# Kernel optimization log

Measured on AMD Instinct MI355X. Metric: run time of the kernel, lower is better.

Reference implementation:

```python
import jax, jax.numpy as jnp
import numpy as np

T, B, FEAT, HID, NCLS = 256, 64, 256, 1024, 257


def hamilton_block(W):
    # W: [4, di, do] components (r,i,j,k) -> full real block matrix [4*di, 4*do]
    Wr, Wi, Wj, Wk = W[0], W[1], W[2], W[3]
    row0 = jnp.concatenate([Wr, Wi, Wj, Wk], axis=-1)
    row1 = jnp.concatenate([-Wi, Wr, -Wk, Wj], axis=-1)
    row2 = jnp.concatenate([-Wj, Wk, Wr, -Wi], axis=-1)
    row3 = jnp.concatenate([-Wk, -Wj, Wi, Wr], axis=-1)
    return jnp.concatenate([row0, row1, row2, row3], axis=-2)


def setup_inputs() -> dict:
    key = jax.random.key(0)
    ks = jax.random.split(key, 7)
    x = jax.random.normal(ks[0], (T, B, FEAT), dtype=jnp.float32)
    sx = 1.0 / np.sqrt(FEAT)
    sh = 1.0 / np.sqrt(HID)
    # 4 gates (f,i,o,c) x 4 quaternion components x [feat/4, hid/4]
    Wx = jax.random.normal(ks[1], (4, 4, FEAT // 4, HID // 4), dtype=jnp.float32) * sx
    bx = jax.random.normal(ks[2], (4, HID), dtype=jnp.float32) * sx
    Wh = jax.random.normal(ks[3], (4, 4, HID // 4, HID // 4), dtype=jnp.float32) * sh
    Wo = jax.random.normal(ks[4], (HID, NCLS), dtype=jnp.float32) * sh
    bo = jax.random.normal(ks[5], (NCLS,), dtype=jnp.float32) * sh
    return {"x": x, "Wx": Wx, "bx": bx, "Wh": Wh, "Wo": Wo, "bo": bo}


def reference(x, Wx, bx, Wh, Wo, bo):
    # Build full real Hamilton-product matrices per gate.
    Wx_full = jax.vmap(hamilton_block)(Wx)  # [4, FEAT, HID]
    Wh_full = jax.vmap(hamilton_block)(Wh)  # [4, HID, HID]
    # Precompute input-to-hidden gate terms for all timesteps: [4, T, B, HID]
    gx = jnp.einsum('tbf,gfh->gtbh', x, Wx_full) + bx[:, None, None, :]

    def step(carry, gx_t):  # gx_t: [4, B, HID]
        h, c = carry
        gh = jnp.einsum('bh,gho->gbo', h, Wh_full)  # [4, B, HID]
        ft = jax.nn.sigmoid(gx_t[0] + gh[0])
        it = jax.nn.sigmoid(gx_t[1] + gh[1])
        ot = jax.nn.sigmoid(gx_t[2] + gh[2])
        at = gx_t[3] + gh[3]
        c = it * jnp.tanh(at) + ft * c
        h = ot * jnp.tanh(c)
        return (h, c), h

    h0 = jnp.zeros((B, HID), dtype=x.dtype)
    _, hs = jax.lax.scan(step, (h0, h0), jnp.moveaxis(gx, 1, 0))  # hs: [T, B, HID]
    return jnp.einsum('tbh,hc->tbc', hs, Wo) + bo  # [T, B, NCLS]
```

## Files before the change

kernel.cpp:

```cpp
#include <hip/hip_runtime.h>
#include <hip/hip_bf16.h>
#include <math.h>

#define T 256
#define B 64
#define FEAT 256
#define HID 1024
#define NCLS 257
#define NCH 4
#define NCG 64
#define NBLK 256
#define NTHR 512
#define HSLOT 16384
#define XSLOT 4096

typedef __attribute__((ext_vector_type(8))) short short8v;
typedef __attribute__((ext_vector_type(4))) float floatx4;

__device__ __constant__ int   d_comp[4][4] = {{0,1,2,3},{1,0,3,2},{2,3,0,1},{3,2,1,0}};
__device__ __constant__ float d_sign[4][4] = {{ 1.f, 1.f, 1.f, 1.f},
                                              {-1.f, 1.f,-1.f, 1.f},
                                              {-1.f, 1.f, 1.f,-1.f},
                                              {-1.f,-1.f, 1.f, 1.f}};

__device__ __forceinline__ ushort f2bf(float f) {
    union { float f; unsigned u; } v; v.f = f;
    unsigned r = v.u + 0x7FFF + ((v.u >> 16) & 1);
    return (ushort)(r >> 16);
}

__device__ __forceinline__ float sigm(float v) { return 1.f / (1.f + __expf(-v)); }
__device__ __forceinline__ float tanh_fast(float v) { return 1.f - 2.f / (1.f + __expf(2.f * v)); }

__global__ __launch_bounds__(256) void conv_xpanel(const float* __restrict__ x,
                                                   ushort* __restrict__ xp) {
    int i = blockIdx.x * 256 + threadIdx.x;
    int k4 = i & 63, b = (i >> 6) & 63, t = i >> 12;
    int k = k4 * 4;
    int c = b >> 4, b16 = b & 15;
    float4 v = ((const float4*)x)[i];
    ushort4 o;
    o.x = f2bf(v.x); o.y = f2bf(v.y); o.z = f2bf(v.z); o.w = f2bf(v.w);
    *(ushort4*)(xp + (size_t)(t * 4 + c) * XSLOT + (k >> 3) * 128 + b16 * 8 + (k & 7)) = o;
}

__global__ __launch_bounds__(256) void prep_wcf(const float* __restrict__ Wh,
                                                const float* __restrict__ Wx,
                                                ushort* __restrict__ wcf) {
    int e = blockIdx.x * 256 + threadIdx.x;
    int j    = e & 7;
    int lane = (e >> 3) & 63;
    int r    = e >> 9;
    int ks   = r % 40;
    int s    = r / 40;
    int mt   = s & 3;
    int cg   = s >> 2;
    int c  = mt * 16 + (lane & 15);
    int hl = c >> 2, g = c & 3;
    int n  = cg * 16 + hl;
    int qq = n >> 8, bc = n & 255;
    int k  = ks * 32 + ((lane >> 4) << 3) + j;
    float v;
    if (k < HID) {
        int p = k >> 8, a = k & 255;
        v = d_sign[p][qq] * Wh[((g * 4 + d_comp[p][qq]) * 256 + a) * 256 + bc];
    } else {
        int kk = k - HID;
        int p = kk >> 6, a = kk & 63;
        v = d_sign[p][qq] * Wx[((g * 4 + d_comp[p][qq]) * 64 + a) * 256 + bc];
    }
    wcf[e] = f2bf(v);
}

__global__ __launch_bounds__(256) void prep_wof(const float* __restrict__ Wo,
                                                ushort* __restrict__ wof) {
    int e = blockIdx.x * 256 + threadIdx.x;
    int j    = e & 7;
    int lane = (e >> 3) & 63;
    int ks   = (e >> 9) & 31;
    int tile = e >> 14;
    int n = tile * 16 + (lane & 15);
    int k = ks * 32 + ((lane >> 4) << 3) + j;
    wof[e] = (n < NCLS) ? f2bf(Wo[k * NCLS + n]) : (ushort)0;
}

__global__ __launch_bounds__(256) void init_hf(ushort* __restrict__ hpan,
                                               uint* __restrict__ flg) {
    int i = blockIdx.x * 256 + threadIdx.x;
    ((ushort4*)hpan)[i] = make_ushort4(0, 0, 0, 0);
    if (blockIdx.x == 0) flg[threadIdx.x] = 0;
}

__global__ __launch_bounds__(512, 2) void qlstm_persist(
    const ushort* __restrict__ xp,
    const ushort* __restrict__ wcf,
    const float*  __restrict__ bx,
    ushort*       __restrict__ hpan,
    uint*         __restrict__ flg)
{
    __shared__ float pre[2][16][72];

    const int tid  = threadIdx.x;
    const int blk  = blockIdx.x;
    const int ch   = blk & 3;
    const int cg   = blk >> 2;
    const int w    = tid >> 6;
    const int lane = tid & 63;
    const int mt   = w & 3;
    const int kh   = w >> 2;
    const int ld_off = (lane >> 4) * 128 + (lane & 15) * 8;

    const ushort* wbase = wcf + ((size_t)(cg * 4 + mt) * 40 + kh * 20) * 512 + lane * 8;
    short8v A[20];
    #pragma unroll
    for (int i = 0; i < 20; ++i) {
        const ushort* ap = wbase + i * 512;
        asm volatile("global_load_dwordx4 %0, %1, off" : "=v"(A[i]) : "v"(ap));
    }
    asm volatile("s_waitcnt vmcnt(0)" ::: "memory");
    __builtin_amdgcn_sched_barrier(0);

    const int gb = tid >> 4;
    const int hl = tid & 15;
    const int gn = cg * 16 + hl;
    float bxf = 0.f, bxi = 0.f, bxo = 0.f, bxa = 0.f;
    if (tid < 256) {
        bxf = bx[gn]; bxi = bx[HID + gn];
        bxo = bx[2 * HID + gn]; bxa = bx[3 * HID + gn];
    }
    float c_reg = 0.f;
    const int st_off = (cg * 2 + (hl >> 3)) * 128 + gb * 8 + (hl & 7);
    uint* myflags = flg + ch * 64;

    for (int t = 0; t < T; ++t) {
        const ushort* hs = hpan + (size_t)(t * NCH + ch) * HSLOT;
        const ushort* xs = xp   + (size_t)(t * NCH + ch) * XSLOT;

        short8v Bf[20];
        if (kh == 1) {
            #pragma unroll
            for (int i = 12; i < 20; ++i) {
                const ushort* p = xs + (i - 12) * 512 + ld_off;
                asm volatile("global_load_dwordx4 %0, %1, off" : "=v"(Bf[i]) : "v"(p));
            }
        }

        if (t > 0) {
            if (w == 0) {
                const uint tgt = (uint)t;
                for (;;) {
                    uint f = __hip_atomic_load(myflags + lane, __ATOMIC_RELAXED,
                                               __HIP_MEMORY_SCOPE_AGENT);
                    if (__all(f >= tgt)) break;
                    __builtin_amdgcn_s_sleep(1);
                }
            }
            __syncthreads();
        }

        if (kh == 0) {
            #pragma unroll
            for (int i = 0; i < 20; ++i) {
                const ushort* p = hs + i * 512 + ld_off;
                asm volatile("global_load_dwordx4 %0, %1, off" : "=v"(Bf[i]) : "v"(p));
            }
        } else {
            #pragma unroll
            for (int i = 0; i < 12; ++i) {
                const ushort* p = hs + (20 + i) * 512 + ld_off;
                asm volatile("global_load_dwordx4 %0, %1, off" : "=v"(Bf[i]) : "v"(p));
            }
        }
        asm volatile("s_waitcnt vmcnt(0)" ::: "memory");
        __builtin_amdgcn_sched_barrier(0);

        floatx4 a0 = {0.f,0.f,0.f,0.f}, a1 = {0.f,0.f,0.f,0.f};
        #pragma unroll
        for (int i = 0; i < 20; i += 2) {
            a0 = __builtin_amdgcn_mfma_f32_16x16x32_bf16(A[i],     Bf[i],     a0, 0, 0, 0);
            a1 = __builtin_amdgcn_mfma_f32_16x16x32_bf16(A[i + 1], Bf[i + 1], a1, 0, 0, 0);
        }
        floatx4 acc = a0 + a1;

        {
            float4 v = make_float4(acc[0], acc[1], acc[2], acc[3]);
            *(float4*)&pre[kh][lane & 15][mt * 16 + (lane >> 4) * 4] = v;
        }
        __syncthreads();

        if (tid < 256) {
            float4 p0 = *(const float4*)&pre[0][gb][hl * 4];
            float4 p1 = *(const float4*)&pre[1][gb][hl * 4];
            float f  = sigm(p0.x + p1.x + bxf);
            float i_ = sigm(p0.y + p1.y + bxi);
            float o  = sigm(p0.z + p1.z + bxo);
            float a  = p0.w + p1.w + bxa;
            c_reg = i_ * tanh_fast(a) + f * c_reg;
            float h = o * tanh_fast(c_reg);
            uint hvu = f2bf(h);
            ushort* hp = hpan + (size_t)((t + 1) * NCH + ch) * HSLOT + st_off;
            asm volatile("global_store_short %0, %1, off sc0 sc1"
                         :: "v"(hp), "v"(hvu) : "memory");
            asm volatile("s_waitcnt vmcnt(0)" ::: "memory");
        }
        __syncthreads();

        if (tid == 0)
            __hip_atomic_store(myflags + cg, (uint)(t + 1),
                               __ATOMIC_RELAXED, __HIP_MEMORY_SCOPE_AGENT);
    }
}

__global__ __launch_bounds__(256) void outproj(const ushort* __restrict__ hpan,
                                               const ushort* __restrict__ wof,
                                               const float* __restrict__ bo,
                                               float* __restrict__ out) {
    const int tt   = blockIdx.x;
    const int nt   = blockIdx.y;
    const int tid  = threadIdx.x;
    const int g    = tid >> 6;
    const int lane = tid & 63;
    const ushort* abase = hpan + ((size_t)(tt + 1) * 4 + g) * HSLOT
                          + (lane >> 4) * 128 + (lane & 15) * 8;
    const short8v* wb = (const short8v*)wof;

    floatx4 ac[4] = {{0.f,0.f,0.f,0.f},{0.f,0.f,0.f,0.f},
                     {0.f,0.f,0.f,0.f},{0.f,0.f,0.f,0.f}};
    #pragma unroll 4
    for (int ks = 0; ks < 32; ++ks) {
        short8v av = *(const short8v*)(abase + ks * 512);
        #pragma unroll
        for (int ct = 0; ct < 4; ++ct)
            ac[ct] = __builtin_amdgcn_mfma_f32_16x16x32_bf16(
                av, wb[((nt * 4 + ct) * 32 + ks) * 64 + lane], ac[ct], 0, 0, 0);
    }
    const int orow = tt * 64 + g * 16 + (lane >> 4) * 4;
    #pragma unroll
    for (int ct = 0; ct < 4; ++ct) {
        int n = nt * 64 + ct * 16 + (lane & 15);
        if (n < NCLS) {
            float bias = bo[n];
            #pragma unroll
            for (int j = 0; j < 4; ++j)
                out[(size_t)(orow + j) * NCLS + n] = ac[ct][j] + bias;
        }
    }
}

extern "C" void kernel_launch(void* const* d_in, const int* in_sizes, int n_in,
                              void* d_out, int out_size, void* d_ws, size_t ws_size,
                              hipStream_t stream) {
    const float* x  = (const float*)d_in[0];
    const float* Wx = (const float*)d_in[1];
    const float* bx = (const float*)d_in[2];
    const float* Wh = (const float*)d_in[3];
    const float* Wo = (const float*)d_in[4];
    const float* bo = (const float*)d_in[5];
    float* out = (float*)d_out;

    ushort* xp   = (ushort*)d_ws;
    ushort* wcf  = xp  + (size_t)T * 4 * XSLOT;
    ushort* wof  = wcf + (size_t)64 * 4 * 40 * 512;
    ushort* hpan = wof + 327680;
    uint*   flg  = (uint*)(hpan + (size_t)(T + 1) * 4 * HSLOT);

    conv_xpanel<<<(T * B * FEAT / 4) / 256, 256, 0, stream>>>(x, xp);
    prep_wcf<<<(64 * 4 * 40 * 512) / 256, 256, 0, stream>>>(Wh, Wx, wcf);
    prep_wof<<<(20 * 32 * 512) / 256, 256, 0, stream>>>(Wo, wof);
    init_hf<<<64, 256, 0, stream>>>(hpan, flg);

    void* args[] = {(void*)&xp, (void*)&wcf, (void*)&bx, (void*)&hpan, (void*)&flg};
    hipLaunchCooperativeKernel((void*)qlstm_persist, dim3(NBLK), dim3(NTHR),
                               args, 0, stream);

    outproj<<<dim3(T, 5), 256, 0, stream>>>(hpan, wof, bo, out);
}
```

Baseline: 1.108 ms.

## Replace block-level flag barrier with per-wave byte flags polled by every wave

Each wave that writes h now publishes its own byte flag, and every wave polls the 256-byte flag row for its channel with one 16-byte load, instead of wave 0 polling then a block barrier. The x-projection MFMAs are split out and issued before the wait, so they overlap the dependency stall. The pre buffer is double-buffered by time parity so the trailing __syncthreads can be dropped. The intent is to cut synchronization latency on the recurrent critical path. In exchange every wave spins on global memory, and the wrapping byte counters with no trailing barrier need care to stay correct.

```diff
diff --git a/kernel.cpp b/kernel.cpp
--- a/kernel.cpp
+++ b/kernel.cpp
@@ -8,7 +8,6 @@
 #define HID 1024
 #define NCLS 257
 #define NCH 4
-#define NCG 64
 #define NBLK 256
 #define NTHR 512
 #define HSLOT 16384
@@ -85,20 +84,26 @@
 }
 
 __global__ __launch_bounds__(256) void init_hf(ushort* __restrict__ hpan,
-                                               uint* __restrict__ flg) {
+                                               unsigned char* __restrict__ flg) {
     int i = blockIdx.x * 256 + threadIdx.x;
     ((ushort4*)hpan)[i] = make_ushort4(0, 0, 0, 0);
-    if (blockIdx.x == 0) flg[threadIdx.x] = 0;
-}
+    if (blockIdx.x == 0 && threadIdx.x < 64)
+        ((uint4*)flg)[threadIdx.x] = make_uint4(0, 0, 0, 0);
+}
+
+#define LOADX4SC(dst, addr) \
+    asm volatile("global_load_dwordx4 %0, %1, off sc0 sc1" : "=v"(dst) : "v"(addr))
+#define LOADX4(dst, addr) \
+    asm volatile("global_load_dwordx4 %0, %1, off" : "=v"(dst) : "v"(addr))
 
 __global__ __launch_bounds__(512, 2) void qlstm_persist(
     const ushort* __restrict__ xp,
     const ushort* __restrict__ wcf,
     const float*  __restrict__ bx,
     ushort*       __restrict__ hpan,
-    uint*         __restrict__ flg)
+    unsigned char* __restrict__ flg)
 {
-    __shared__ float pre[2][16][72];
+    __shared__ float pre[2][2][16][72];
 
     const int tid  = threadIdx.x;
     const int blk  = blockIdx.x;
@@ -108,15 +113,14 @@
     const int lane = tid & 63;
     const int mt   = w & 3;
     const int kh   = w >> 2;
-    const int ld_off = (lane >> 4) * 128 + (lane & 15) * 8;
-
-    const ushort* wbase = wcf + ((size_t)(cg * 4 + mt) * 40 + kh * 20) * 512 + lane * 8;
-    short8v A[20];
+    const int lofs = (lane >> 4) * 128 + (lane & 15) * 8;
+
+    const ushort* wbase = wcf + (size_t)(cg * 4 + mt) * 40 * 512 + lane * 8;
+    short8v A[16], Ax[4];
     #pragma unroll
-    for (int i = 0; i < 20; ++i) {
-        const ushort* ap = wbase + i * 512;
-        asm volatile("global_load_dwordx4 %0, %1, off" : "=v"(A[i]) : "v"(ap));
-    }
+    for (int i = 0; i < 16; ++i) LOADX4(A[i], wbase + (kh * 16 + i) * 512);
+    #pragma unroll
+    for (int u = 0; u < 4; ++u)  LOADX4(Ax[u], wbase + (32 + kh * 4 + u) * 512);
     asm volatile("s_waitcnt vmcnt(0)" ::: "memory");
     __builtin_amdgcn_sched_barrier(0);
 
@@ -130,67 +134,60 @@
     }
     float c_reg = 0.f;
     const int st_off = (cg * 2 + (hl >> 3)) * 128 + gb * 8 + (hl & 7);
-    uint* myflags = flg + ch * 64;
+    const uint* pollp = (const uint*)(flg + ch * 256) + (lane & 15) * 4;
+    unsigned char* myflag = flg + ch * 256 + w * 64 + cg;
 
     for (int t = 0; t < T; ++t) {
         const ushort* hs = hpan + (size_t)(t * NCH + ch) * HSLOT;
         const ushort* xs = xp   + (size_t)(t * NCH + ch) * XSLOT;
-
-        short8v Bf[20];
-        if (kh == 1) {
-            #pragma unroll
-            for (int i = 12; i < 20; ++i) {
-                const ushort* p = xs + (i - 12) * 512 + ld_off;
-                asm volatile("global_load_dwordx4 %0, %1, off" : "=v"(Bf[i]) : "v"(p));
-            }
-        }
-
-        if (t > 0) {
-            if (w == 0) {
-                const uint tgt = (uint)t;
-                for (;;) {
-                    uint f = __hip_atomic_load(myflags + lane, __ATOMIC_RELAXED,
-                                               __HIP_MEMORY_SCOPE_AGENT);
-                    if (__all(f >= tgt)) break;
-                    __builtin_amdgcn_s_sleep(1);
-                }
-            }
-            __syncthreads();
-        }
-
-        if (kh == 0) {
-            #pragma unroll
-            for (int i = 0; i < 20; ++i) {
-                const ushort* p = hs + i * 512 + ld_off;
-                asm volatile("global_load_dwordx4 %0, %1, off" : "=v"(Bf[i]) : "v"(p));
-            }
-        } else {
-            #pragma unroll
-            for (int i = 0; i < 12; ++i) {
-                const ushort* p = hs + (20 + i) * 512 + ld_off;
-                asm volatile("global_load_dwordx4 %0, %1, off" : "=v"(Bf[i]) : "v"(p));
-            }
-        }
+        const int par = t & 1;
+
+        short8v xv[4];
+        #pragma unroll
+        for (int u = 0; u < 4; ++u) LOADX4(xv[u], xs + (kh * 4 + u) * 512 + lofs);
         asm volatile("s_waitcnt vmcnt(0)" ::: "memory");
         __builtin_amdgcn_sched_barrier(0);
-
         floatx4 a0 = {0.f,0.f,0.f,0.f}, a1 = {0.f,0.f,0.f,0.f};
-        #pragma unroll
-        for (int i = 0; i < 20; i += 2) {
-            a0 = __builtin_amdgcn_mfma_f32_16x16x32_bf16(A[i],     Bf[i],     a0, 0, 0, 0);
-            a1 = __builtin_amdgcn_mfma_f32_16x16x32_bf16(A[i + 1], Bf[i + 1], a1, 0, 0, 0);
+        a0 = __builtin_amdgcn_mfma_f32_16x16x32_bf16(Ax[0], xv[0], a0, 0, 0, 0);
+        a1 = __builtin_amdgcn_mfma_f32_16x16x32_bf16(Ax[1], xv[1], a1, 0, 0, 0);
+        a0 = __builtin_amdgcn_mfma_f32_16x16x32_bf16(Ax[2], xv[2], a0, 0, 0, 0);
+        a1 = __builtin_amdgcn_mfma_f32_16x16x32_bf16(Ax[3], xv[3], a1, 0, 0, 0);
+
+        if (t > 0) {
+            const uint rep = (uint)(((t - 1) & 127) + 1) * 0x01010101u;
+            for (;;) {
+                uint4 F;
+                LOADX4SC(F, pollp);
+                asm volatile("s_waitcnt vmcnt(0)" ::: "memory");
+                if (__all((F.x == rep) && (F.y == rep) &&
+                          (F.z == rep) && (F.w == rep))) break;
+                __builtin_amdgcn_s_sleep(1);
+            }
+        }
+
+        short8v Bh[16];
+        #pragma unroll
+        for (int i = 0; i < 16; ++i)
+            LOADX4SC(Bh[i], hs + (kh * 16 + i) * 512 + lofs);
+        asm volatile("s_waitcnt vmcnt(0)" ::: "memory");
+        __builtin_amdgcn_sched_barrier(0);
+
+        #pragma unroll
+        for (int i = 0; i < 16; i += 2) {
+            a0 = __builtin_amdgcn_mfma_f32_16x16x32_bf16(A[i],     Bh[i],     a0, 0, 0, 0);
+            a1 = __builtin_amdgcn_mfma_f32_16x16x32_bf16(A[i + 1], Bh[i + 1], a1, 0, 0, 0);
         }
         floatx4 acc = a0 + a1;
 
         {
             float4 v = make_float4(acc[0], acc[1], acc[2], acc[3]);
-            *(float4*)&pre[kh][lane & 15][mt * 16 + (lane >> 4) * 4] = v;
+            *(float4*)&pre[par][kh][lane & 15][mt * 16 + (lane >> 4) * 4] = v;
         }
         __syncthreads();
 
         if (tid < 256) {
-            float4 p0 = *(const float4*)&pre[0][gb][hl * 4];
-            float4 p1 = *(const float4*)&pre[1][gb][hl * 4];
+            float4 p0 = *(const float4*)&pre[par][0][gb][hl * 4];
+            float4 p1 = *(const float4*)&pre[par][1][gb][hl * 4];
             float f  = sigm(p0.x + p1.x + bxf);
             float i_ = sigm(p0.y + p1.y + bxi);
             float o  = sigm(p0.z + p1.z + bxo);
@@ -202,12 +199,12 @@
             asm volatile("global_store_short %0, %1, off sc0 sc1"
                          :: "v"(hp), "v"(hvu) : "memory");
             asm volatile("s_waitcnt vmcnt(0)" ::: "memory");
-        }
-        __syncthreads();
-
-        if (tid == 0)
-            __hip_atomic_store(myflags + cg, (uint)(t + 1),
-                               __ATOMIC_RELAXED, __HIP_MEMORY_SCOPE_AGENT);
+            if (lane == 0) {
+                uint fv = (uint)((t & 127) + 1);
+                asm volatile("global_store_byte %0, %1, off sc0 sc1"
+                             :: "v"(myflag), "v"(fv) : "memory");
+            }
+        }
     }
 }
 
@@ -262,7 +259,7 @@
     ushort* wcf  = xp  + (size_t)T * 4 * XSLOT;
     ushort* wof  = wcf + (size_t)64 * 4 * 40 * 512;
     ushort* hpan = wof + 327680;
-    uint*   flg  = (uint*)(hpan + (size_t)(T + 1) * 4 * HSLOT);
+    unsigned char* flg = (unsigned char*)(hpan + (size_t)(T + 1) * 4 * HSLOT);
 
     conv_xpanel<<<(T * B * FEAT / 4) / 256, 256, 0, stream>>>(x, xp);
     prep_wcf<<<(64 * 4 * 40 * 512) / 256, 256, 0, stream>>>(Wh, Wx, wcf);
```

Result: slower. 2.842 ms (+156.6%).
